# Kernel tuning notes

Measured on AMD Instinct MI355X. Metric: run time of the kernel, lower is better.

The kernel has to match this reference:

```python
import jax, jax.numpy as jnp
import numpy as np

E = 128       # embed_dim
H = 128       # hidden_dim
NLABEL = 5
VOCAB = 50000
DEPTH = 18    # levels 0..17, complete binary tree
BRANCH = 2
N_NODES = 2 ** DEPTH - 1  # level-order layout: level l occupies [2^l-1, 2^(l+1)-1)


def setup_inputs() -> dict:
    key = jax.random.key(0)
    ks = jax.random.split(key, 24)

    def w(k, shape):
        return jax.random.normal(k, shape, dtype=jnp.float32) * 0.05

    inp = {
        "embeds": w(ks[0], (VOCAB, E)),
        "node_words": jax.random.randint(ks[1], (N_NODES,), 0, VOCAB),
        "node_labels": jax.random.randint(ks[2], (N_NODES,), 0, NLABEL),
        "depth": DEPTH,
        "branching": BRANCH,
    }
    # 8 gate linears: *x maps E->H, *h maps H->H (torch nn.Linear: y = x @ W.T + b)
    for j, nm in enumerate(["ix", "ih", "fx", "fh", "ox", "oh", "ux", "uh"]):
        in_dim = E if nm.endswith("x") else H
        inp["W" + nm] = w(ks[3 + 2 * j], (H, in_dim))
        inp["b" + nm] = w(ks[4 + 2 * j], (H,))
    inp["Wout"] = w(ks[20], (NLABEL, H))
    inp["bout"] = w(ks[21], (NLABEL,))
    return inp


def _lin(x, W, b):
    return x @ W.T + b


def _tree_lstm(embeds, node_words, node_labels, depth, branching,
               Wix, bix, Wih, bih, Wfx, bfx, Wfh, bfh,
               Wox, box, Woh, boh, Wux, bux, Wuh, buh, Wout, bout):
    b = branching
    hid = Wix.shape[0]
    loss = jnp.zeros((), dtype=embeds.dtype)
    child_c = child_h = None
    logp = None
    # bottom-up over levels (leaves first); level l has b^l nodes at offset (b^l-1)/(b-1)
    for l in range(depth - 1, -1, -1):
        n = b ** l
        off = (b ** l - 1) // (b - 1)
        x = embeds[node_words[off:off + n]]            # [n, E]
        if child_h is None:                            # leaves: zero child states
            h_sum = jnp.zeros((n, hid), dtype=embeds.dtype)
            c_agg = jnp.zeros((n, hid), dtype=embeds.dtype)
        else:
            ch = child_h.reshape(n, b, hid)            # children of each level-l node
            cc = child_c.reshape(n, b, hid)
            h_sum = ch.sum(axis=1)                     # child-sum
            f = jax.nn.sigmoid(_lin(x, Wfx, bfx)[:, None, :] + _lin(ch, Wfh, bfh))
            c_agg = (f * cc).sum(axis=1)               # sum_k f_k * c_k
        i = jax.nn.sigmoid(_lin(x, Wix, bix) + _lin(h_sum, Wih, bih))
        o = jax.nn.sigmoid(_lin(x, Wox, box) + _lin(h_sum, Woh, boh))
        u = jnp.tanh(_lin(x, Wux, bux) + _lin(h_sum, Wuh, buh))
        c = i * u + c_agg
        h = o * jnp.tanh(c)
        logp = jax.nn.log_softmax(_lin(h, Wout, bout), axis=-1)   # [n, NLABEL]
        lab = node_labels[off:off + n]
        loss = loss - logp[jnp.arange(n), lab].sum()              # NLL summed over nodes
        child_c, child_h = c, h
    return logp, loss  # logp from level 0 = root log-probs [1, NLABEL]


def reference(embeds, node_words, node_labels, depth, branching,
              Wix, bix, Wih, bih, Wfx, bfx, Wfh, bfh,
              Wox, box, Woh, boh, Wux, bux, Wuh, buh, Wout, bout):
    return _tree_lstm(embeds, node_words, node_labels, depth, branching,
                      Wix, bix, Wih, bih, Wfx, bfx, Wfh, bfh,
                      Wox, box, Woh, boh, Wux, bux, Wuh, buh, Wout, bout)
```

## Files before the change

### kernel.cpp

```cpp
#include <hip/hip_runtime.h>
#include <math.h>

#define DEPTH 18
#define NINT ((1 << (DEPTH - 1)) - 1)
#define LEAF_OFF ((1 << (DEPTH - 2)) - 1)
#define NVOCAB 50000
#define SAW 520
#define KTS 9

typedef unsigned short bf16raw;
typedef __bf16 bf16x8 __attribute__((ext_vector_type(8)));
typedef float f32x4 __attribute__((ext_vector_type(4)));
typedef short short8 __attribute__((ext_vector_type(8)));

__device__ __forceinline__ float sigm(float x) { return 1.0f / (1.0f + __expf(-x)); }
__device__ __forceinline__ float fast_tanh(float x) {
    float t = __expf(2.0f * x);
    return 1.0f - 2.0f / (t + 1.0f);
}

__device__ __forceinline__ float bf2f(bf16raw u) {
    union { unsigned int i; float f; } v;
    v.i = ((unsigned int)u) << 16;
    return v.f;
}
__device__ __forceinline__ bf16raw f2bf(float f) {
    union { float f; unsigned int i; } v;
    v.f = f;
    unsigned int r = v.i + 0x7FFFu + ((v.i >> 16) & 1u);
    return (bf16raw)(r >> 16);
}

#define SB() __builtin_amdgcn_sched_barrier(0)

__global__ __launch_bounds__(256) void k_prep_embeds(const float* __restrict__ src,
                                                     bf16raw* __restrict__ dst, int n4)
{
    int i = blockIdx.x * blockDim.x + threadIdx.x;
    if (i < n4) {
        float4 v = ((const float4*)src)[i];
        ushort4 o;
        o.x = f2bf(v.x); o.y = f2bf(v.y); o.z = f2bf(v.z); o.w = f2bf(v.w);
        ((ushort4*)dst)[i] = o;
    }
}

__global__ __launch_bounds__(128) void k_prep_bcat(
    const float* __restrict__ Wix, const float* __restrict__ bix,
    const float* __restrict__ Wih, const float* __restrict__ bih,
    const float* __restrict__ Wfx, const float* __restrict__ bfx,
    const float* __restrict__ Wfh, const float* __restrict__ bfh,
    const float* __restrict__ Wox, const float* __restrict__ box_,
    const float* __restrict__ Woh, const float* __restrict__ boh,
    const float* __restrict__ Wux, const float* __restrict__ bux,
    const float* __restrict__ Wuh, const float* __restrict__ buh,
    bf16raw* __restrict__ Bfrag, float* __restrict__ bias_cat)
{
    const int j = blockIdx.x;
    const int gate = j >> 7, jj = j & 127;
    const float *Wx, *Wh, *bx, *bh;
    switch (gate) {
        case 0: Wx = Wix; Wh = Wih; bx = bix;  bh = bih; break;
        case 1: Wx = Wux; Wh = Wuh; bx = bux;  bh = buh; break;
        case 2: Wx = Wox; Wh = Woh; bx = box_; bh = boh; break;
        default: Wx = Wfx; Wh = Wfh; bx = bfx; bh = bfh; break;
    }
    const int coltile = (j >> 4) & 7, lr = j & 15;
    for (int k = threadIdx.x; k < 256; k += blockDim.x) {
        float v = (k < 128) ? Wx[jj * 128 + k] : Wh[jj * 128 + (k - 128)];
        const int idx = (((gate * 8 + coltile) * KTS + (k >> 5)) * 64
                         + ((k >> 3) & 3) * 16 + lr) * 8 + (k & 7);
        Bfrag[idx] = f2bf(v);
    }
    if (threadIdx.x == 0) bias_cat[j] = bx[jj] + bh[jj];
}

template<int CB>
__device__ __forceinline__ void lp_burst(const bf16raw* __restrict__ bfbase, int wcol,
                                         bf16x8 (&bb)[16])
{
#pragma unroll
    for (int kt = 0; kt < 4; ++kt)
#pragma unroll
        for (int j = 0; j < 4; ++j)
            bb[kt * 4 + j] = *(const bf16x8*)(bfbase +
                    (long)(((CB * 8 + (wcol >> 4) + j) * KTS + kt) * 512));
}

__device__ __forceinline__ void lp_mfma_all(const bf16raw* __restrict__ sA, int wrow,
                                            int lrow, int lquad,
                                            bf16x8 (&bb)[16], f32x4 (&acc)[2][4])
{
#pragma unroll
    for (int kt = 0; kt < 4; ++kt) {
        bf16x8 af[2];
#pragma unroll
        for (int i = 0; i < 2; ++i)
            af[i] = *(const bf16x8*)&sA[(wrow + i * 16 + lrow) * 136 + kt * 32 + lquad * 8];
#pragma unroll
        for (int i = 0; i < 2; ++i)
#pragma unroll
            for (int j = 0; j < 4; ++j)
                acc[i][j] = __builtin_amdgcn_mfma_f32_16x16x32_bf16(af[i], bb[kt * 4 + j], acc[i][j], 0, 0, 0);
    }
}

template<int CB>
__device__ __forceinline__ void lp_rungemm(const bf16raw* __restrict__ sA,
                                           const bf16raw* __restrict__ bfbase,
                                           int wrow, int wcol, int lrow, int lquad,
                                           f32x4 (&acc)[2][4])
{
#pragma unroll
    for (int i = 0; i < 2; i++)
#pragma unroll
        for (int j = 0; j < 4; j++) acc[i][j] = (f32x4){0.f, 0.f, 0.f, 0.f};
    bf16x8 bb[16];
    lp_burst<CB>(bfbase, wcol, bb);
    SB();
    lp_mfma_all(sA, wrow, lrow, lquad, bb, acc);
}

template<int G, int H>
__device__ __forceinline__ void load8(const bf16raw* __restrict__ bfbase, int w,
                                      bf16x8 (&bb)[8])
{
#pragma unroll
    for (int kt2 = 0; kt2 < 4; ++kt2)
#pragma unroll
        for (int jj = 0; jj < 2; ++jj)
            bb[kt2 * 2 + jj] = *(const bf16x8*)(bfbase +
                    (long)(((G * 8 + w * 2 + jj) * KTS + H * 4 + kt2) * 512));
}

template<int PASS, int H>
__device__ __forceinline__ void mfma8(const bf16raw* __restrict__ sA, int lrow, int lquad,
                                      bf16x8 (&bb)[8], f32x4 (&acc)[2][2])
{
    constexpr int base = (PASS == 2) ? (H ? 8 : 0)
                       : (PASS == 3) ? (H ? 12 : 0)
                       : H * 4;
#pragma unroll
    for (int kt2 = 0; kt2 < 4; ++kt2) {
        bf16x8 af[2];
#pragma unroll
        for (int i = 0; i < 2; ++i)
            af[i] = *(const bf16x8*)&sA[(i * 16 + lrow) * SAW + (base + kt2) * 32 + lquad * 8];
#pragma unroll
        for (int jj = 0; jj < 2; ++jj)
#pragma unroll
            for (int i = 0; i < 2; ++i)
                acc[i][jj] = __builtin_amdgcn_mfma_f32_16x16x32_bf16(af[i], bb[kt2 * 2 + jj], acc[i][jj], 0, 0, 0);
    }
}

__global__ __launch_bounds__(256, 3) void k_leafpre(
    const bf16raw* __restrict__ embeds_bf,
    const bf16raw* __restrict__ Bfrag, const float* __restrict__ bias_cat,
    const float* __restrict__ Wout, const float* __restrict__ bout,
    bf16raw* __restrict__ hc_leaf, float* __restrict__ lossv6, int nvtot)
{
    const int vbase = blockIdx.x * 64;
    int nv = nvtot - vbase;
    if (nv > 64) nv = 64;
    if (nv <= 0) return;

    __shared__ __align__(16) bf16raw sA[64 * 136];
    __shared__ __align__(16) bf16raw sT[64 * 136];
    __shared__ float sWout[5 * 128];

    const int t = threadIdx.x;
    for (int i = t; i < 640; i += 256) sWout[i] = Wout[i];

    {
        const int row = t >> 2;
        const int co = (t & 3) * 32;
        const int arow = (row < nv) ? row : 0;
        const bf16raw* ax = embeds_bf + (long)(vbase + arow) * 128;
        *(short8*)&sA[row * 136 + co]      = *(const short8*)(ax + co);
        *(short8*)&sA[row * 136 + co + 8]  = *(const short8*)(ax + co + 8);
        *(short8*)&sA[row * 136 + co + 16] = *(const short8*)(ax + co + 16);
        *(short8*)&sA[row * 136 + co + 24] = *(const short8*)(ax + co + 24);
    }

    const int lane = t & 63;
    const int w = t >> 6;
    const int wrow = (w & 1) * 32;
    const int wcol = (w >> 1) * 64;
    const int lrow = lane & 15;
    const int lquad = lane >> 4;

    __syncthreads();

    const bf16raw* bfbase = Bfrag + (long)lane * 8;

    float tval[2][4][4];
    f32x4 acc[2][4];

    lp_rungemm<0>(sA, bfbase, wrow, wcol, lrow, lquad, acc);
#pragma unroll
    for (int i = 0; i < 2; i++)
#pragma unroll
        for (int jj = 0; jj < 4; jj++) {
            const float b = bias_cat[wcol + jj * 16 + lrow];
#pragma unroll
            for (int r = 0; r < 4; r++) tval[i][jj][r] = sigm(acc[i][jj][r] + b);
        }
    lp_rungemm<1>(sA, bfbase, wrow, wcol, lrow, lquad, acc);
#pragma unroll
    for (int i = 0; i < 2; i++)
#pragma unroll
        for (int jj = 0; jj < 4; jj++) {
            const float b = bias_cat[128 + wcol + jj * 16 + lrow];
#pragma unroll
            for (int r = 0; r < 4; r++) tval[i][jj][r] *= fast_tanh(acc[i][jj][r] + b);
        }
#pragma unroll
    for (int i = 0; i < 2; i++)
#pragma unroll
        for (int jj = 0; jj < 4; jj++)
#pragma unroll
            for (int r = 0; r < 4; r++) {
                const int m = wrow + i * 16 + lquad * 4 + r;
                const int j = wcol + jj * 16 + lrow;
                sT[m * 136 + j] = f2bf(tval[i][jj][r]);
            }
#pragma unroll
    for (int i = 0; i < 2; i++)
#pragma unroll
        for (int jj = 0; jj < 4; jj++)
#pragma unroll
            for (int r = 0; r < 4; r++) tval[i][jj][r] = fast_tanh(tval[i][jj][r]);
    __syncthreads();
#pragma unroll
    for (int s = 0; s < 4; ++s) {
        int ci = t + 256 * s;
        int row = ci >> 4, c8 = (ci & 15) * 8;
        if (row < nv)
            *(short8*)(hc_leaf + (long)(vbase + row) * 256 + 128 + c8) = *(const short8*)&sT[row * 136 + c8];
    }
    lp_rungemm<2>(sA, bfbase, wrow, wcol, lrow, lquad, acc);
    __syncthreads();
#pragma unroll
    for (int i = 0; i < 2; i++)
#pragma unroll
        for (int jj = 0; jj < 4; jj++) {
            const float b = bias_cat[256 + wcol + jj * 16 + lrow];
#pragma unroll
            for (int r = 0; r < 4; r++) {
                const int m = wrow + i * 16 + lquad * 4 + r;
                const int j = wcol + jj * 16 + lrow;
                sT[m * 136 + j] = f2bf(sigm(acc[i][jj][r] + b) * tval[i][jj][r]);
            }
        }
    __syncthreads();
#pragma unroll
    for (int s = 0; s < 4; ++s) {
        int ci = t + 256 * s;
        int row = ci >> 4, c8 = (ci & 15) * 8;
        if (row < nv)
            *(short8*)(hc_leaf + (long)(vbase + row) * 256 + c8) = *(const short8*)&sT[row * 136 + c8];
    }
    {
        const int row = t >> 2, q = t & 3;
        float p[5] = {0.f, 0.f, 0.f, 0.f, 0.f};
        for (int k0 = 0; k0 < 32; ++k0) {
            const int k = q * 32 + k0;
            float hv = bf2f(sT[row * 136 + k]);
#pragma unroll
            for (int l = 0; l < 5; l++) p[l] += hv * sWout[l * 128 + k];
        }
#pragma unroll
        for (int l = 0; l < 5; l++) {
            p[l] += __shfl_down(p[l], 2);
            p[l] += __shfl_down(p[l], 1);
        }
        if (q == 0 && row < nv) {
            float lg[5], mx = -1e30f;
#pragma unroll
            for (int l = 0; l < 5; l++) {
                lg[l] = p[l] + bout[l];
                mx = fmaxf(mx, lg[l]);
            }
            float se = 0.f;
#pragma unroll
            for (int l = 0; l < 5; l++) se += __expf(lg[l] - mx);
            float lse = __logf(se) + mx;
            float* dst = lossv6 + (long)(vbase + row) * 6;
#pragma unroll
            for (int l = 0; l < 5; l++) dst[l] = lg[l];
            dst[5] = lse;
        }
    }
}

__global__ __launch_bounds__(256, 3) void k_level32(
    const bf16raw* __restrict__ embeds_bf, const int* __restrict__ words,
    bf16raw* __restrict__ h_all, bf16raw* __restrict__ c_all,
    const bf16raw* __restrict__ hc_leaf,
    const bf16raw* __restrict__ Bfrag, const float* __restrict__ bias_cat,
    int off, int nm, int leafkids)
{
    __shared__ __align__(16) bf16raw sA[32 * SAW];
    __shared__ __align__(16) bf16raw sCT[64 * 136];

    const int t = threadIdx.x;
    const int m0 = blockIdx.x * 32;

    {
        const int row = t >> 3;
        const int co = (t & 7) * 8;
        int mm = m0 + row; if (mm >= nm) mm = nm - 1;
        const long g = (long)off + mm;
        const bf16raw* px = embeds_bf + (long)words[g] * 128;
        const bf16raw *p1, *p2;
        if (leafkids) {
            p1 = hc_leaf + (long)words[2 * g + 1] * 256;
            p2 = hc_leaf + (long)words[2 * g + 2] * 256;
        } else {
            p1 = h_all + (2 * g + 1) * 128;
            p2 = h_all + (2 * g + 2) * 128;
        }
        short8 vx0 = *(const short8*)(px + co);
        short8 vx1 = *(const short8*)(px + 64 + co);
        short8 h10 = *(const short8*)(p1 + co);
        short8 h11 = *(const short8*)(p1 + 64 + co);
        short8 h20 = *(const short8*)(p2 + co);
        short8 h21 = *(const short8*)(p2 + 64 + co);
        short8 hs0, hs1;
#pragma unroll
        for (int e = 0; e < 8; ++e) {
            hs0[e] = (short)f2bf(bf2f((bf16raw)(unsigned short)h10[e]) +
                                 bf2f((bf16raw)(unsigned short)h20[e]));
            hs1[e] = (short)f2bf(bf2f((bf16raw)(unsigned short)h11[e]) +
                                 bf2f((bf16raw)(unsigned short)h21[e]));
        }
        *(short8*)&sA[row * SAW + co]        = vx0;
        *(short8*)&sA[row * SAW + 64 + co]   = vx1;
        *(short8*)&sA[row * SAW + 128 + co]  = hs0;
        *(short8*)&sA[row * SAW + 192 + co]  = hs1;
        *(short8*)&sA[row * SAW + 256 + co]  = h10;
        *(short8*)&sA[row * SAW + 320 + co]  = h11;
        *(short8*)&sA[row * SAW + 384 + co]  = h20;
        *(short8*)&sA[row * SAW + 448 + co]  = h21;
    }
    {
        const int slot = t >> 2;
        const int cc8 = (t & 3) * 8;
        int mm = m0 + (slot >> 1); if (mm >= nm) mm = nm - 1;
        const long g = (long)off + mm;
        const long cg = 2 * g + 1 + (slot & 1);
        const bf16raw* pc = leafkids ? (hc_leaf + (long)words[cg] * 256 + 128)
                                     : (c_all + cg * 128);
#pragma unroll
        for (int s = 0; s < 4; ++s)
            *(short8*)&sCT[slot * 136 + s * 32 + cc8] = *(const short8*)(pc + s * 32 + cc8);
    }

    const int lane = t & 63;
    const int w = t >> 6;
    const int lrow = lane & 15;
    const int lquad = lane >> 4;

    float bias[4][2];
#pragma unroll
    for (int g = 0; g < 4; ++g)
#pragma unroll
        for (int jj = 0; jj < 2; ++jj)
            bias[g][jj] = bias_cat[g * 128 + w * 32 + jj * 16 + lrow];

    __syncthreads();

    const bf16raw* bfbase = Bfrag + (long)lane * 8;

    f32x4 acc[2][2];
    float si[2][2][4];
    float cc[2][2][4];
    float hh[2][2][4];
    bf16x8 bbA[8], bbB[8];

#define ZACC() { _Pragma("unroll") for (int i_ = 0; i_ < 2; ++i_) \
                 _Pragma("unroll") for (int j_ = 0; j_ < 2; ++j_) \
                     acc[i_][j_] = (f32x4){0.f, 0.f, 0.f, 0.f}; }

    load8<0, 0>(bfbase, w, bbA);
    load8<0, 1>(bfbase, w, bbB);
    SB();
    ZACC();
    mfma8<0, 0>(sA, lrow, lquad, bbA, acc); SB();
    load8<1, 0>(bfbase, w, bbA); SB();
    mfma8<0, 1>(sA, lrow, lquad, bbB, acc); SB();
    load8<1, 1>(bfbase, w, bbB); SB();
#pragma unroll
    for (int i = 0; i < 2; ++i)
#pragma unroll
        for (int jj = 0; jj < 2; ++jj)
#pragma unroll
            for (int r = 0; r < 4; ++r)
                si[i][jj][r] = sigm(acc[i][jj][r] + bias[0][jj]);
    ZACC();
    mfma8<1, 0>(sA, lrow, lquad, bbA, acc); SB();
    load8<3, 0>(bfbase, w, bbA); SB();
    mfma8<1, 1>(sA, lrow, lquad, bbB, acc); SB();
    load8<3, 1>(bfbase, w, bbB); SB();
#pragma unroll
    for (int i = 0; i < 2; ++i)
#pragma unroll
        for (int jj = 0; jj < 2; ++jj)
#pragma unroll
            for (int r = 0; r < 4; ++r)
                cc[i][jj][r] = si[i][jj][r] * fast_tanh(acc[i][jj][r] + bias[1][jj]);
    ZACC();
    mfma8<2, 0>(sA, lrow, lquad, bbA, acc);
    mfma8<2, 1>(sA, lrow, lquad, bbB, acc);
    SB();
#pragma unroll
    for (int i = 0; i < 2; ++i)
#pragma unroll
        for (int jj = 0; jj < 2; ++jj) {
            const int j = w * 32 + jj * 16 + lrow;
#pragma unroll
            for (int r = 0; r < 4; ++r) {
                const int m = i * 16 + lquad * 4 + r;
                cc[i][jj][r] += sigm(acc[i][jj][r] + bias[3][jj]) * bf2f(sCT[(2 * m) * 136 + j]);
            }
        }
    ZACC();
    mfma8<3, 0>(sA, lrow, lquad, bbA, acc);
    mfma8<3, 1>(sA, lrow, lquad, bbB, acc);
    SB();
    load8<2, 0>(bfbase, w, bbA);
    load8<2, 1>(bfbase, w, bbB);
    SB();
#pragma unroll
    for (int i = 0; i < 2; ++i)
#pragma unroll
        for (int jj = 0; jj < 2; ++jj) {
            const int j = w * 32 + jj * 16 + lrow;
#pragma unroll
            for (int r = 0; r < 4; ++r) {
                const int m = i * 16 + lquad * 4 + r;
                cc[i][jj][r] += sigm(acc[i][jj][r] + bias[3][jj]) * bf2f(sCT[(2 * m + 1) * 136 + j]);
            }
        }
    ZACC();
    mfma8<4, 0>(sA, lrow, lquad, bbA, acc);
    mfma8<4, 1>(sA, lrow, lquad, bbB, acc);
    SB();
#pragma unroll
    for (int i = 0; i < 2; ++i)
#pragma unroll
        for (int jj = 0; jj < 2; ++jj)
#pragma unroll
            for (int r = 0; r < 4; ++r)
                hh[i][jj][r] = sigm(acc[i][jj][r] + bias[2][jj]) * fast_tanh(cc[i][jj][r]);
#undef ZACC

    __syncthreads();

#pragma unroll
    for (int i = 0; i < 2; ++i)
#pragma unroll
        for (int jj = 0; jj < 2; ++jj) {
            const int j = w * 32 + jj * 16 + lrow;
#pragma unroll
            for (int r = 0; r < 4; ++r) {
                const int m = i * 16 + lquad * 4 + r;
                sCT[m * 136 + j] = f2bf(cc[i][jj][r]);
                sCT[(32 + m) * 136 + j] = f2bf(hh[i][jj][r]);
            }
        }
    __syncthreads();

#pragma unroll
    for (int q = 0; q < 4; ++q) {
        int ci = t + 256 * q;
        int row = ci >> 4;
        int c8 = (ci & 15) * 8;
        int m = row & 31;
        if (m0 + m < nm) {
            bf16raw* dst = (row < 32) ? c_all : h_all;
            *(short8*)(dst + ((long)off + m0 + m) * 128 + c8) = *(const short8*)&sCT[row * 136 + c8];
        }
    }
}

__global__ __launch_bounds__(256) void k_loss(
    const bf16raw* __restrict__ h_all, const int* __restrict__ words,
    const int* __restrict__ labels, const float* __restrict__ lossv6,
    const float* __restrict__ Wout, const float* __restrict__ bout,
    float* __restrict__ partials, float* __restrict__ out)
{
    __shared__ float sWout[640];
    __shared__ float red[128];
    const int t = threadIdx.x;
    for (int i = t; i < 640; i += 256) sWout[i] = Wout[i];

    const int row = t >> 1, half = t & 1;
    const long g = (long)blockIdx.x * 128 + row;
    const bool valid = g < NINT;
    const long gg = valid ? g : 0;
    __syncthreads();

    float p[5] = {0.f, 0.f, 0.f, 0.f, 0.f};
    const bf16raw* hp = h_all + gg * 128 + half * 64;
#pragma unroll
    for (int s = 0; s < 8; ++s) {
        short8 v = *(const short8*)(hp + s * 8);
#pragma unroll
        for (int e = 0; e < 8; ++e) {
            float hv = bf2f((bf16raw)(unsigned short)v[e]);
#pragma unroll
            for (int l = 0; l < 5; l++) p[l] += hv * sWout[l * 128 + half * 64 + s * 8 + e];
        }
    }
#pragma unroll
    for (int l = 0; l < 5; l++) p[l] += __shfl_down(p[l], 1);

    float lossNode = 0.f;
    if (half == 0 && valid) {
        float lg[5], mx = -1e30f;
#pragma unroll
        for (int l = 0; l < 5; l++) {
            lg[l] = p[l] + bout[l];
            mx = fmaxf(mx, lg[l]);
        }
        float se = 0.f;
#pragma unroll
        for (int l = 0; l < 5; l++) se += __expf(lg[l] - mx);
        float lse = __logf(se) + mx;
        lossNode = lse - lg[labels[gg]];
        if (gg >= LEAF_OFF) {
            const float* lv1 = lossv6 + (long)words[2 * gg + 1] * 6;
            const float* lv2 = lossv6 + (long)words[2 * gg + 2] * 6;
            lossNode += (lv1[5] - lv1[labels[2 * gg + 1]])
                      + (lv2[5] - lv2[labels[2 * gg + 2]]);
        }
        if (gg == 0) {
#pragma unroll
            for (int l = 0; l < 5; l++) out[l] = lg[l] - lse;
        }
    }
    if (half == 0) red[row] = lossNode;
    __syncthreads();
    if (t < 64) {
        float s = red[t] + red[t + 64];
#pragma unroll
        for (int d = 32; d > 0; d >>= 1) s += __shfl_down(s, d);
        if (t == 0) atomicAdd(&partials[blockIdx.x & 1023], s);
    }
}

__global__ __launch_bounds__(256) void k3_reduce(const float* __restrict__ partials,
                                                 float* __restrict__ out)
{
    const int t = threadIdx.x;
    float s = 0.f;
    for (int i = t; i < 1024; i += 256) s += partials[i];
#pragma unroll
    for (int d = 32; d > 0; d >>= 1) s += __shfl_down(s, d);
    __shared__ float red[4];
    if ((t & 63) == 0) red[t >> 6] = s;
    __syncthreads();
    if (t == 0) out[5] = red[0] + red[1] + red[2] + red[3];
}

extern "C" void kernel_launch(void* const* d_in, const int* in_sizes, int n_in,
                              void* d_out, int out_size, void* d_ws, size_t ws_size,
                              hipStream_t stream)
{
    const float* embeds = (const float*)d_in[0];
    const int* words = (const int*)d_in[1];
    const int* labels = (const int*)d_in[2];
    const float* Wix = (const float*)d_in[5],  *bix  = (const float*)d_in[6];
    const float* Wih = (const float*)d_in[7],  *bih  = (const float*)d_in[8];
    const float* Wfx = (const float*)d_in[9],  *bfx  = (const float*)d_in[10];
    const float* Wfh = (const float*)d_in[11], *bfh  = (const float*)d_in[12];
    const float* Wox = (const float*)d_in[13], *box_ = (const float*)d_in[14];
    const float* Woh = (const float*)d_in[15], *boh  = (const float*)d_in[16];
    const float* Wux = (const float*)d_in[17], *bux  = (const float*)d_in[18];
    const float* Wuh = (const float*)d_in[19], *buh  = (const float*)d_in[20];
    const float* Wout = (const float*)d_in[21], *bout = (const float*)d_in[22];
    float* out = (float*)d_out;

    char* ws = (char*)d_ws;
    const size_t treeElems = (size_t)NINT * 128;
    bf16raw* h_all = (bf16raw*)ws;
    bf16raw* c_all = h_all + treeElems;
    bf16raw* embeds_bf = c_all + treeElems;
    bf16raw* Bfrag = embeds_bf + (size_t)NVOCAB * 128;
    bf16raw* hc_leaf = Bfrag + 4 * 8 * KTS * 512;
    float* lossv6 = (float*)(hc_leaf + (size_t)NVOCAB * 256);
    float* bias_cat = lossv6 + (size_t)NVOCAB * 6;
    float* partials = bias_cat + 512;

    k_prep_embeds<<<(NVOCAB * 128 / 4 + 255) / 256, 256, 0, stream>>>(
        embeds, embeds_bf, NVOCAB * 128 / 4);
    k_prep_bcat<<<512, 128, 0, stream>>>(Wix, bix, Wih, bih, Wfx, bfx, Wfh, bfh,
                                         Wox, box_, Woh, boh, Wux, bux, Wuh, buh,
                                         Bfrag, bias_cat);
    hipMemsetAsync(partials, 0, 1024 * sizeof(float), stream);

    k_leafpre<<<(NVOCAB + 63) / 64, 256, 0, stream>>>(
        embeds_bf, Bfrag, bias_cat, Wout, bout, hc_leaf, lossv6, NVOCAB);

    for (int l = DEPTH - 2; l >= 0; --l) {
        const int n = 1 << l;
        k_level32<<<dim3((n + 31) / 32), 256, 0, stream>>>(
            embeds_bf, words, h_all, c_all, hc_leaf, Bfrag, bias_cat,
            n - 1, n, (l == DEPTH - 2) ? 1 : 0);
    }

    k_loss<<<(NINT + 127) / 128, 256, 0, stream>>>(
        h_all, words, labels, lossv6, Wout, bout, partials, out);
    k3_reduce<<<1, 256, 0, stream>>>(partials, out);
}
```

Before: 372.2 us.

## Fuse small upper tree levels into one cooperative kernel with grid sync

Levels 10 down to 0 of the tree, where each level is small, now run inside a single cooperative kernel of 32 blocks that steps through the levels with grid.sync barriers, replacing eleven separate launches. The intent is to remove launch overhead and idle gaps on the latency-bound top of the tree. The level body is factored into a device function, and the MFMA order for the forget gate is changed so the shared x-part is computed once and reused for both children. The trade-off is that the cooperative launch and grid barriers have their own cost, and only 32 blocks handle level 10.

```diff
diff --git a/kernel.cpp b/kernel.cpp
--- a/kernel.cpp
+++ b/kernel.cpp
@@ -1,5 +1,8 @@
 #include <hip/hip_runtime.h>
+#include <hip/hip_cooperative_groups.h>
 #include <math.h>
+
+namespace cg = cooperative_groups;
 
 #define DEPTH 18
 #define NINT ((1 << (DEPTH - 1)) - 1)
@@ -133,19 +136,16 @@
                     (long)(((G * 8 + w * 2 + jj) * KTS + H * 4 + kt2) * 512));
 }
 
-template<int PASS, int H>
-__device__ __forceinline__ void mfma8(const bf16raw* __restrict__ sA, int lrow, int lquad,
-                                      bf16x8 (&bb)[8], f32x4 (&acc)[2][2])
-{
-    constexpr int base = (PASS == 2) ? (H ? 8 : 0)
-                       : (PASS == 3) ? (H ? 12 : 0)
-                       : H * 4;
+template<int AB>
+__device__ __forceinline__ void mfma4k(const bf16raw* __restrict__ sA, int lrow, int lquad,
+                                       bf16x8 (&bb)[8], f32x4 (&acc)[2][2])
+{
 #pragma unroll
     for (int kt2 = 0; kt2 < 4; ++kt2) {
         bf16x8 af[2];
 #pragma unroll
         for (int i = 0; i < 2; ++i)
-            af[i] = *(const bf16x8*)&sA[(i * 16 + lrow) * SAW + (base + kt2) * 32 + lquad * 8];
+            af[i] = *(const bf16x8*)&sA[(i * 16 + lrow) * SAW + (AB + kt2) * 32 + lquad * 8];
 #pragma unroll
         for (int jj = 0; jj < 2; ++jj)
 #pragma unroll
@@ -294,18 +294,16 @@
     }
 }
 
-__global__ __launch_bounds__(256, 3) void k_level32(
+__device__ __forceinline__ void level_body(
     const bf16raw* __restrict__ embeds_bf, const int* __restrict__ words,
     bf16raw* __restrict__ h_all, bf16raw* __restrict__ c_all,
     const bf16raw* __restrict__ hc_leaf,
     const bf16raw* __restrict__ Bfrag, const float* __restrict__ bias_cat,
-    int off, int nm, int leafkids)
-{
-    __shared__ __align__(16) bf16raw sA[32 * SAW];
-    __shared__ __align__(16) bf16raw sCT[64 * 136];
-
+    bf16raw* sA, bf16raw* sCT,
+    int off, int m0, int nm, int leafkids)
+{
     const int t = threadIdx.x;
-    const int m0 = blockIdx.x * 32;
+    __syncthreads();
 
     {
         const int row = t >> 3;
@@ -374,6 +372,7 @@
     const bf16raw* bfbase = Bfrag + (long)lane * 8;
 
     f32x4 acc[2][2];
+    f32x4 fx[2][2];
     float si[2][2][4];
     float cc[2][2][4];
     float hh[2][2][4];
@@ -387,9 +386,9 @@
     load8<0, 1>(bfbase, w, bbB);
     SB();
     ZACC();
-    mfma8<0, 0>(sA, lrow, lquad, bbA, acc); SB();
+    mfma4k<0>(sA, lrow, lquad, bbA, acc); SB();
     load8<1, 0>(bfbase, w, bbA); SB();
-    mfma8<0, 1>(sA, lrow, lquad, bbB, acc); SB();
+    mfma4k<4>(sA, lrow, lquad, bbB, acc); SB();
     load8<1, 1>(bfbase, w, bbB); SB();
 #pragma unroll
     for (int i = 0; i < 2; ++i)
@@ -399,9 +398,9 @@
             for (int r = 0; r < 4; ++r)
                 si[i][jj][r] = sigm(acc[i][jj][r] + bias[0][jj]);
     ZACC();
-    mfma8<1, 0>(sA, lrow, lquad, bbA, acc); SB();
+    mfma4k<0>(sA, lrow, lquad, bbA, acc); SB();
     load8<3, 0>(bfbase, w, bbA); SB();
-    mfma8<1, 1>(sA, lrow, lquad, bbB, acc); SB();
+    mfma4k<4>(sA, lrow, lquad, bbB, acc); SB();
     load8<3, 1>(bfbase, w, bbB); SB();
 #pragma unroll
     for (int i = 0; i < 2; ++i)
@@ -411,8 +410,15 @@
             for (int r = 0; r < 4; ++r)
                 cc[i][jj][r] = si[i][jj][r] * fast_tanh(acc[i][jj][r] + bias[1][jj]);
     ZACC();
-    mfma8<2, 0>(sA, lrow, lquad, bbA, acc);
-    mfma8<2, 1>(sA, lrow, lquad, bbB, acc);
+    mfma4k<0>(sA, lrow, lquad, bbA, acc);
+    SB();
+#pragma unroll
+    for (int i = 0; i < 2; ++i)
+#pragma unroll
+        for (int jj = 0; jj < 2; ++jj) fx[i][jj] = acc[i][jj];
+    mfma4k<8>(sA, lrow, lquad, bbB, acc);
+    SB();
+    load8<2, 0>(bfbase, w, bbA);
     SB();
 #pragma unroll
     for (int i = 0; i < 2; ++i)
@@ -425,11 +431,12 @@
                 cc[i][jj][r] += sigm(acc[i][jj][r] + bias[3][jj]) * bf2f(sCT[(2 * m) * 136 + j]);
             }
         }
-    ZACC();
-    mfma8<3, 0>(sA, lrow, lquad, bbA, acc);
-    mfma8<3, 1>(sA, lrow, lquad, bbB, acc);
-    SB();
-    load8<2, 0>(bfbase, w, bbA);
+#pragma unroll
+    for (int i = 0; i < 2; ++i)
+#pragma unroll
+        for (int jj = 0; jj < 2; ++jj) acc[i][jj] = fx[i][jj];
+    mfma4k<12>(sA, lrow, lquad, bbB, acc);
+    SB();
     load8<2, 1>(bfbase, w, bbB);
     SB();
 #pragma unroll
@@ -444,8 +451,8 @@
             }
         }
     ZACC();
-    mfma8<4, 0>(sA, lrow, lquad, bbA, acc);
-    mfma8<4, 1>(sA, lrow, lquad, bbB, acc);
+    mfma4k<0>(sA, lrow, lquad, bbA, acc);
+    mfma4k<4>(sA, lrow, lquad, bbB, acc);
     SB();
 #pragma unroll
     for (int i = 0; i < 2; ++i)
@@ -482,6 +489,38 @@
             bf16raw* dst = (row < 32) ? c_all : h_all;
             *(short8*)(dst + ((long)off + m0 + m) * 128 + c8) = *(const short8*)&sCT[row * 136 + c8];
         }
+    }
+}
+
+__global__ __launch_bounds__(256, 3) void k_level32(
+    const bf16raw* __restrict__ embeds_bf, const int* __restrict__ words,
+    bf16raw* __restrict__ h_all, bf16raw* __restrict__ c_all,
+    const bf16raw* __restrict__ hc_leaf,
+    const bf16raw* __restrict__ Bfrag, const float* __restrict__ bias_cat,
+    int off, int nm, int leafkids)
+{
+    __shared__ __align__(16) bf16raw sA[32 * SAW];
+    __shared__ __align__(16) bf16raw sCT[64 * 136];
+    level_body(embeds_bf, words, h_all, c_all, hc_leaf, Bfrag, bias_cat,
+               sA, sCT, off, blockIdx.x * 32, nm, leafkids);
+}
+
+__global__ __launch_bounds__(256, 3) void k_level_coop(
+    const bf16raw* embeds_bf, const int* words,
+    bf16raw* h_all, bf16raw* c_all,
+    const bf16raw* hc_leaf,
+    const bf16raw* Bfrag, const float* bias_cat)
+{
+    __shared__ __align__(16) bf16raw sA[32 * SAW];
+    __shared__ __align__(16) bf16raw sCT[64 * 136];
+    cg::grid_group grid = cg::this_grid();
+    for (int l = 10; l >= 0; --l) {
+        const int n = 1 << l;
+        for (int m0 = (int)blockIdx.x * 32; m0 < n; m0 += (int)gridDim.x * 32)
+            level_body(embeds_bf, words, h_all, c_all, hc_leaf, Bfrag, bias_cat,
+                       sA, sCT, n - 1, m0, n, 0);
+        __threadfence();
+        grid.sync();
     }
 }
 
@@ -604,12 +643,24 @@
     k_leafpre<<<(NVOCAB + 63) / 64, 256, 0, stream>>>(
         embeds_bf, Bfrag, bias_cat, Wout, bout, hc_leaf, lossv6, NVOCAB);
 
-    for (int l = DEPTH - 2; l >= 0; --l) {
+    for (int l = DEPTH - 2; l >= 11; --l) {
         const int n = 1 << l;
         k_level32<<<dim3((n + 31) / 32), 256, 0, stream>>>(
             embeds_bf, words, h_all, c_all, hc_leaf, Bfrag, bias_cat,
             n - 1, n, (l == DEPTH - 2) ? 1 : 0);
     }
+    {
+        const bf16raw* a0 = embeds_bf;
+        const int* a1 = words;
+        bf16raw* a2 = h_all;
+        bf16raw* a3 = c_all;
+        const bf16raw* a4 = hc_leaf;
+        const bf16raw* a5 = Bfrag;
+        const float* a6 = bias_cat;
+        void* cargs[] = { &a0, &a1, &a2, &a3, &a4, &a5, &a6 };
+        hipLaunchCooperativeKernel((void*)k_level_coop, dim3(32), dim3(256),
+                                   cargs, 0, stream);
+    }
 
     k_loss<<<(NINT + 127) / 128, 256, 0, stream>>>(
         h_all, words, labels, lossv6, Wout, bout, partials, out);
```

Result: slower. 583.6 us (+56.8%).
